# Optimization experiments

Measured on AMD Instinct MI355X. Metric: run time of the kernel, lower is better.

The kernel has to match this reference:

```python
import jax, jax.numpy as jnp
import numpy as np

N_NONZERO = 32      # n_nonzero_coefs
TAU = 0.01
LAMBDA_INIT = -5.0  # reg_coeff = softplus(lambda)


def setup_inputs() -> dict:
    key = jax.random.key(0)
    k1, k2 = jax.random.split(key)
    X = jax.random.normal(k1, (64, 1024, 1024), dtype=jnp.float32)
    y = jax.random.normal(k2, (64, 1024, 1), dtype=jnp.float32)
    return {"X": X, "y": y}


def _omp_fit_forward(X, y):
    # Faithful translation of fit() (omp with hard straight-through top-1)
    # followed by forward() reconstruction D @ coef.
    reg = jax.nn.softplus(jnp.asarray(LAMBDA_INIT, jnp.float32)).astype(X.dtype)
    B, L, A = X.shape
    ones = jnp.ones((B, L, 1), X.dtype)
    Dfull = jnp.concatenate([X, ones], axis=-1)   # [B, L, A+1] (bias column)
    D = Dfull[0]                                   # shared dictionary [L, A+1]
    n_atoms = A + 1
    y2 = y[:, :, 0]                                # [B, L]
    y_det = jax.lax.stop_gradient(y2)
    residuals = y_det
    # Cache selected_D columns incrementally: each column j is dict @ ret_j,
    # identical math to the original's full recompute every iteration.
    selD = jnp.zeros((B, L, N_NONZERO), X.dtype)
    idx_all = []
    nzW = None
    for i in range(N_NONZERO):
        proj = residuals @ D                                      # [B, A+1]
        soft = jax.nn.softmax(jnp.abs(proj) / TAU, axis=-1)
        idx = jnp.argmax(jnp.abs(proj), axis=-1)                  # detached indices
        onehot = jax.nn.one_hot(jnp.argmax(soft, axis=-1), n_atoms, dtype=X.dtype)
        ret = onehot - jax.lax.stop_gradient(soft) + soft         # straight-through
        new_col = ret @ D.T                                       # [B, L]
        selD = selD.at[:, :, i].set(new_col)
        Di = selD[:, :, :i + 1]                                   # [B, L, i+1]
        DTy = jnp.einsum('blk,bl->bk', Di, y2)[..., None]         # [B, i+1, 1]
        DTD = jnp.einsum('blk,blj->bkj', Di, Di) + reg * jnp.eye(i + 1, dtype=X.dtype)
        nzW = jnp.linalg.solve(DTD, DTy)                          # [B, i+1, 1]
        residuals = y_det - jnp.einsum('blk,bk->bl', Di, nzW[..., 0])
        idx_all.append(idx)
    indices = jnp.stack(idx_all, axis=1)                          # [B, K] int
    W = jnp.zeros((B, n_atoms), X.dtype).at[jnp.arange(B)[:, None], indices].set(nzW[..., 0])
    # forward(): bmm(dict_with_bias, coef)
    recon = jnp.einsum('bla,ba->bl', Dfull, W)[..., None]         # [B, L, 1]
    return recon


def reference(X, y):
    return _omp_fit_forward(X, y)
```

## Files before the change

### kernel.cpp

```cpp
#include <hip/hip_runtime.h>
#include <math.h>

#define NATOMS   1025
#define GSTRIDE  1040
#define GELEMS   (1025*GSTRIDE)
#define NNZ      32
#define NBATCH   64
#define REGL     0.0067153485f

#define DPPF(x, ctrl) __int_as_float(__builtin_amdgcn_update_dpp(0, __float_as_int(x), (ctrl), 0xF, 0xF, false))

__device__ __forceinline__ float wave_max64(float x) {
    x = fmaxf(x, DPPF(x, 0x111));
    x = fmaxf(x, DPPF(x, 0x112));
    x = fmaxf(x, DPPF(x, 0x114));
    x = fmaxf(x, DPPF(x, 0x118));
    x = fmaxf(x, DPPF(x, 0x142));
    x = fmaxf(x, DPPF(x, 0x143));
    return __int_as_float(__builtin_amdgcn_readlane(__float_as_int(x), 63));
}
__device__ __forceinline__ float wave_sum64(float x) {
    x += DPPF(x, 0x111);
    x += DPPF(x, 0x112);
    x += DPPF(x, 0x114);
    x += DPPF(x, 0x118);
    x += DPPF(x, 0x142);
    x += DPPF(x, 0x143);
    return __int_as_float(__builtin_amdgcn_readlane(__float_as_int(x), 63));
}

__global__ __launch_bounds__(256)
void gramprojy_kernel(const float* __restrict__ X0, const float* __restrict__ y,
                      float* __restrict__ Gout, float* __restrict__ PY,
                      int kLen, int nsplit) {
    __shared__ float lds[8192];
    const int tid = threadIdx.x;

    if ((int)blockIdx.z < nsplit) {
        const int bx = blockIdx.x, by = blockIdx.y, bz = blockIdx.z;
        if (by < bx) return;
        float* As = lds;
        float* Bs = lds + 4096;
        const int a0 = bx * 128, b0 = by * 128;
        float* __restrict__ Gp = Gout + (size_t)bz * GELEMS;
        const int tx = tid & 15;
        const int ty = tid >> 4;
        const int lr = tid >> 5;
        const int lc = (tid & 31) * 4;
        const bool aIn = (a0 + 128) <= 1024;
        const bool bIn = (b0 + 128) <= 1024;

        float acc[8][8];
#pragma unroll
        for (int m = 0; m < 8; ++m)
#pragma unroll
            for (int n = 0; n < 8; ++n) acc[m][n] = 0.0f;

        const int kBase = bz * kLen;
        for (int kc = 0; kc < kLen; kc += 32) {
#pragma unroll
            for (int rr = 0; rr < 4; ++rr) {
                const int r = lr + rr * 8;
                const int l = kBase + kc + r;
                if (aIn) {
                    *(float4*)&As[r * 128 + lc] = *(const float4*)&X0[(size_t)l * 1024 + a0 + lc];
                } else {
#pragma unroll
                    for (int k = 0; k < 4; ++k) {
                        const int col = a0 + lc + k;
                        As[r * 128 + lc + k] = (col < 1024) ? X0[(size_t)l * 1024 + col]
                                                            : (col == 1024 ? 1.0f : 0.0f);
                    }
                }
                if (bIn) {
                    *(float4*)&Bs[r * 128 + lc] = *(const float4*)&X0[(size_t)l * 1024 + b0 + lc];
                } else {
#pragma unroll
                    for (int k = 0; k < 4; ++k) {
                        const int col = b0 + lc + k;
                        Bs[r * 128 + lc + k] = (col < 1024) ? X0[(size_t)l * 1024 + col]
                                                            : (col == 1024 ? 1.0f : 0.0f);
                    }
                }
            }
            __syncthreads();
#pragma unroll 8
            for (int l = 0; l < 32; ++l) {
                float4 a01 = *(const float4*)&As[l * 128 + ty * 8];
                float4 a23 = *(const float4*)&As[l * 128 + ty * 8 + 4];
                float4 bA  = *(const float4*)&Bs[l * 128 + tx * 4];
                float4 bB  = *(const float4*)&Bs[l * 128 + 64 + tx * 4];
                float am[8] = {a01.x, a01.y, a01.z, a01.w, a23.x, a23.y, a23.z, a23.w};
                float bn[8] = {bA.x, bA.y, bA.z, bA.w, bB.x, bB.y, bB.z, bB.w};
#pragma unroll
                for (int m = 0; m < 8; ++m)
#pragma unroll
                    for (int n = 0; n < 8; ++n)
                        acc[m][n] += am[m] * bn[n];
            }
            __syncthreads();
        }

#pragma unroll
        for (int m = 0; m < 8; ++m) {
            const int a = a0 + ty * 8 + m;
            if (a >= NATOMS) continue;
            const int bAc = b0 + tx * 4;
            const int bBc = b0 + 64 + tx * 4;
            if (bAc < GSTRIDE) {
                *(float4*)&Gp[(size_t)a * GSTRIDE + bAc] =
                    make_float4(acc[m][0], acc[m][1], acc[m][2], acc[m][3]);
            }
            if (bBc < GSTRIDE) {
                *(float4*)&Gp[(size_t)a * GSTRIDE + bBc] =
                    make_float4(acc[m][4], acc[m][5], acc[m][6], acc[m][7]);
            }
        }
    } else {
        const int pw = blockIdx.y * 9 + blockIdx.x;
        if (pw >= 68) return;
        const int a0 = (pw % 17) * 64;
        const int b0 = (pw / 17) * 16;
        float* Ds = lds;
        float* Ys = lds + 2048;
        const int tx = tid & 15;
        const int ty = tid >> 4;
        const bool aIn = (a0 + 64) <= 1024;

        float acc[4] = {0.0f, 0.0f, 0.0f, 0.0f};

        for (int kc = 0; kc < 1024; kc += 32) {
            {
                const int r  = tid >> 4;
                const int c4 = (tid & 15) * 4;
#pragma unroll
                for (int rr = 0; rr < 2; ++rr) {
                    const int row = r + rr * 16;
                    const int l = kc + row;
                    if (aIn) {
                        *(float4*)&Ds[row * 64 + c4] = *(const float4*)&X0[(size_t)l * 1024 + a0 + c4];
                    } else {
#pragma unroll
                        for (int k = 0; k < 4; ++k) {
                            const int col = a0 + c4 + k;
                            Ds[row * 64 + c4 + k] = (col < 1024) ? X0[(size_t)l * 1024 + col]
                                                                 : (col == 1024 ? 1.0f : 0.0f);
                        }
                    }
                }
            }
            for (int e = tid; e < 512; e += 256) {
                const int l = e & 31, bb = e >> 5;
                Ys[l * 17 + bb] = y[(size_t)(b0 + bb) * 1024 + kc + l];
            }
            __syncthreads();
#pragma unroll 8
            for (int l = 0; l < 32; ++l) {
                const float yv = Ys[l * 17 + ty];
                float4 dv = *(const float4*)&Ds[l * 64 + tx * 4];
                acc[0] += yv * dv.x; acc[1] += yv * dv.y;
                acc[2] += yv * dv.z; acc[3] += yv * dv.w;
            }
            __syncthreads();
        }
        const int a = a0 + tx * 4;
        if (a < GSTRIDE) {
            *(float4*)&PY[(size_t)(b0 + ty) * GSTRIDE + a] =
                make_float4(acc[0], acc[1], acc[2], acc[3]);
        }
    }
}

__global__ __launch_bounds__(256)
void combine_kernel(const float* __restrict__ Gp, float* __restrict__ G,
                    float* __restrict__ diagG, int nsplit) {
    int tt = blockIdx.x, bx = 0;
    while (tt >= 9 - bx) { tt -= 9 - bx; ++bx; }
    const int by = bx + tt;
    const int yq = blockIdx.y;
    const int tid = threadIdx.x;
    for (int rep = 0; rep < 16; ++rep) {
        const int idx = yq * 4096 + rep * 256 + tid;
        const int r = idx >> 7, c = idx & 127;
        const int a = bx * 128 + r, b = by * 128 + c;
        if (a > 1024 || b > 1024) continue;
        float s = 0.0f;
        for (int z = 0; z < nsplit; ++z)
            s += Gp[(size_t)z * GELEMS + (size_t)a * GSTRIDE + b];
        G[(size_t)a * GSTRIDE + b] = s;
        G[(size_t)b * GSTRIDE + a] = s;
        if (a == b) diagG[a] = s;
    }
}

__global__ __launch_bounds__(512)
void omp_kernel(const float* __restrict__ G, const float* __restrict__ PY,
                const float* __restrict__ diagG,
                int* __restrict__ idxOut, float* __restrict__ wOut) {
    __shared__ float rowsLds[NNZ][GSTRIDE];
    __shared__ float pyLds[1040];
    __shared__ float diagLds[1040];
    __shared__ float Ainv[32][33];
    __shared__ float wv[32], rhs[32], uvb[32];
    __shared__ int   selIdx[32];
    __shared__ float redV[8];
    __shared__ int   redI[8];
    __shared__ float sc_dinv;

    const int b = blockIdx.x, tid = threadIdx.x;
    const int lane = tid & 63, wid = tid >> 6;

    {
        float4 z4 = make_float4(0.f, 0.f, 0.f, 0.f);
        float4* rz = (float4*)rowsLds;
        for (int u = tid; u < NNZ * GSTRIDE / 4; u += 512) rz[u] = z4;
        if (tid < 32) { wv[tid] = 0.f; rhs[tid] = 0.f; uvb[tid] = 0.f; }
        for (int u = tid; u < 32 * 33; u += 512) ((float*)Ainv)[u] = 0.f;
        const float* pyg = PY + (size_t)b * GSTRIDE;
        for (int u = tid; u < 1040; u += 512) pyLds[u] = pyg[u];
        for (int u = tid; u < 1025; u += 512) diagLds[u] = diagG[u];
    }
    __syncthreads();

    float p0 = pyLds[2 * tid], p1 = pyLds[2 * tid + 1];
    float p2 = (tid == 511) ? pyLds[1024] : 0.0f;

    {
        float best = fabsf(p0); int bidx = 2 * tid;
        { float v = fabsf(p1); if (v > best) { best = v; bidx = 2 * tid + 1; } }
        if (tid == 511) { float v = fabsf(p2); if (v > best) { best = v; bidx = 1024; } }
        const float wmax = wave_max64(best);
        const unsigned long long mask = __ballot(best == wmax);
        const int fl = __ffsll((unsigned long long)mask) - 1;
        const int widx = __builtin_amdgcn_readlane(bidx, fl);
        if (lane == 0) { redV[wid] = wmax; redI[wid] = widx; }
    }
    __syncthreads();

    for (int i = 0; i < NNZ; ++i) {
        float bv_ = redV[0]; int sel = redI[0];
#pragma unroll
        for (int q = 1; q < 8; ++q) {
            if (redV[q] > bv_ || (redV[q] == bv_ && redI[q] < sel)) {
                bv_ = redV[q]; sel = redI[q];
            }
        }
        const float pysel = pyLds[sel];

        float2 rv = make_float2(0.f, 0.f);
        float rv2 = 0.f;
        const float* __restrict__ grow = G + (size_t)sel * GSTRIDE;
        if (i < NNZ - 1) {
            rv = *(const float2*)(grow + 2 * tid);
            if (tid == 511) rv2 = grow[1024];
        }

        if (wid == 0) {
            float bvl = 0.0f, rl = 0.0f;
            if (lane < 32) { bvl = rowsLds[lane][sel]; rl = rhs[lane]; }
            const int lr_ = lane & 31;
            float u0 = 0.f, u1 = 0.f, u2 = 0.f, u3 = 0.f;
#pragma unroll
            for (int m = 0; m < 32; m += 4) {
                u0 = fmaf(Ainv[lr_][m + 0], rowsLds[m + 0][sel], u0);
                u1 = fmaf(Ainv[lr_][m + 1], rowsLds[m + 1][sel], u1);
                u2 = fmaf(Ainv[lr_][m + 2], rowsLds[m + 2][sel], u2);
                u3 = fmaf(Ainv[lr_][m + 3], rowsLds[m + 3][sel], u3);
            }
            const float uacc = (u0 + u1) + (u2 + u3);
            const float t = wave_sum64(bvl * uacc);
            const float s = wave_sum64(rl * uacc);
            const float dinv = 1.0f / (diagLds[sel] + REGL - t);
            const float beta = dinv * (pysel - s);
            if (lane < 32) {
                uvb[lane] = (lane == i) ? -1.0f : uacc;
                wv[lane]  = (lane == i) ? beta  : wv[lane] - uacc * beta;
            }
            if (lane == 0) { selIdx[i] = sel; rhs[i] = pysel; sc_dinv = dinv; }
        }
        __syncthreads();
        if (i == NNZ - 1) break;

        {
            const float dcur = sc_dinv;
            const int e0 = 2 * tid, j0 = e0 >> 5, k0 = e0 & 31;
            Ainv[j0][k0] = fmaf(uvb[j0] * uvb[k0], dcur, Ainv[j0][k0]);
            const int e1 = 2 * tid + 1, j1 = e1 >> 5, k1 = e1 & 31;
            Ainv[j1][k1] = fmaf(uvb[j1] * uvb[k1], dcur, Ainv[j1][k1]);
        }

        const float beta = wv[i];
        float z0 = -rv.x, z1 = -rv.y, z2 = -rv2;
        for (int jb = 0; jb < NNZ; jb += 8) {
            if (jb >= i) break;
#pragma unroll
            for (int jj = 0; jj < 8; ++jj) {
                const int j = jb + jj;
                const float uj = uvb[j];
                z0 = fmaf(uj, rowsLds[j][2 * tid],     z0);
                z1 = fmaf(uj, rowsLds[j][2 * tid + 1], z1);
                if (tid == 511) z2 = fmaf(uj, rowsLds[j][1024], z2);
            }
        }
        p0 = fmaf(beta, z0, p0);
        p1 = fmaf(beta, z1, p1);
        if (tid == 511) p2 = fmaf(beta, z2, p2);

        rowsLds[i][2 * tid]     = rv.x;
        rowsLds[i][2 * tid + 1] = rv.y;
        if (tid == 511) rowsLds[i][1024] = rv2;

        {
            float best = fabsf(p0); int bidx = 2 * tid;
            { float v = fabsf(p1); if (v > best) { best = v; bidx = 2 * tid + 1; } }
            if (tid == 511) { float v = fabsf(p2); if (v > best) { best = v; bidx = 1024; } }
            const float wmax = wave_max64(best);
            const unsigned long long mask = __ballot(best == wmax);
            const int fl = __ffsll((unsigned long long)mask) - 1;
            const int widx = __builtin_amdgcn_readlane(bidx, fl);
            if (lane == 0) { redV[wid] = wmax; redI[wid] = widx; }
        }
        __syncthreads();
    }

    if (tid < NNZ) {
        idxOut[b * NNZ + tid] = selIdx[tid];
        wOut[b * NNZ + tid] = wv[tid];
    }
}

__global__ __launch_bounds__(256)
void recon_kernel(const float* __restrict__ X, const int* __restrict__ idxIn,
                  const float* __restrict__ wIn, float* __restrict__ out) {
    __shared__ float4 Wd4[260];
    const int b = blockIdx.x >> 3, chunk = blockIdx.x & 7;
    const int tid = threadIdx.x, lane = tid & 63, wid = tid >> 6;
    float* Wd = (float*)Wd4;
    for (int u = tid; u < 1040; u += 256) Wd[u] = 0.0f;
    __syncthreads();
    if (tid == 0) {
#pragma unroll
        for (int i = 0; i < NNZ; ++i) Wd[idxIn[b * NNZ + i]] = wIn[b * NNZ + i];
    }
    __syncthreads();
    const float wOne = Wd[1024];
    const float* Xb = X + (size_t)b * 1024 * 1024;

    for (int rr = wid; rr < 128; rr += 4) {
        const int r = chunk * 128 + rr;
        const float4* xr = (const float4*)(Xb + (size_t)r * 1024);
        float acc = 0.0f;
#pragma unroll
        for (int q = 0; q < 4; ++q) {
            float4 x = xr[q * 64 + lane];
            float4 w = Wd4[q * 64 + lane];
            acc += x.x * w.x + x.y * w.y + x.z * w.z + x.w * w.w;
        }
        acc = wave_sum64(acc);
        if (lane == 0) out[(size_t)b * 1024 + r] = acc + wOne;
    }
}

extern "C" void kernel_launch(void* const* d_in, const int* in_sizes, int n_in,
                              void* d_out, int out_size, void* d_ws, size_t ws_size,
                              hipStream_t stream) {
    const float* X = (const float*)d_in[0];
    const float* y = (const float*)d_in[1];
    float* out = (float*)d_out;
    float* ws = (float*)d_ws;

    const size_t need4 = ((size_t)GELEMS * 5 + 64 * GSTRIDE + NBATCH * NNZ * 2 + 2048) * sizeof(float);
    const int nsplit = (ws_size >= need4) ? 4 : 1;
    const int kLen = 1024 / nsplit;

    float* Gp = ws;
    float* G  = ws + (size_t)GELEMS * nsplit;
    float* PY = G + (size_t)GELEMS;
    float* wOut = PY + (size_t)64 * GSTRIDE;
    int* idxOut = (int*)(wOut + NBATCH * NNZ);
    float* diagG = (float*)(idxOut + NBATCH * NNZ);

    gramprojy_kernel<<<dim3(9, 9, nsplit + 1), 256, 0, stream>>>(X, y, Gp, PY, kLen, nsplit);
    combine_kernel<<<dim3(45, 4), 256, 0, stream>>>(Gp, G, diagG, nsplit);
    omp_kernel<<<NBATCH, 512, 0, stream>>>(G, PY, diagG, idxOut, wOut);
    recon_kernel<<<NBATCH * 8, 256, 0, stream>>>(X, idxOut, wOut, out);
}
```

Before: 218.7 us.

## Fuse split-K Gram reduction into OMP row gathers and sparsify reconstruction

Removes the combine kernel. The OMP kernel now sums the split-K partial Gram tiles on the fly, only for the rows it selects and the diagonal, and uses the upper-triangle tile layout to pick an offset. The reconstruction kernel now gathers only the 32 selected columns of X per row, with one thread per row, instead of a dense 1024-wide dot product. This saves a full Gram pass and most of the X read traffic in recon. In exchange, the OMP row loads become nsplit-fold and partly strided (column reads of a row), and the recon gathers from X are uncoalesced.

New measurement: 301.8 us. +38.0%, slower.

```diff
diff --git a/kernel.cpp b/kernel.cpp
--- a/kernel.cpp
+++ b/kernel.cpp
@@ -171,32 +171,9 @@
     }
 }
 
-__global__ __launch_bounds__(256)
-void combine_kernel(const float* __restrict__ Gp, float* __restrict__ G,
-                    float* __restrict__ diagG, int nsplit) {
-    int tt = blockIdx.x, bx = 0;
-    while (tt >= 9 - bx) { tt -= 9 - bx; ++bx; }
-    const int by = bx + tt;
-    const int yq = blockIdx.y;
-    const int tid = threadIdx.x;
-    for (int rep = 0; rep < 16; ++rep) {
-        const int idx = yq * 4096 + rep * 256 + tid;
-        const int r = idx >> 7, c = idx & 127;
-        const int a = bx * 128 + r, b = by * 128 + c;
-        if (a > 1024 || b > 1024) continue;
-        float s = 0.0f;
-        for (int z = 0; z < nsplit; ++z)
-            s += Gp[(size_t)z * GELEMS + (size_t)a * GSTRIDE + b];
-        G[(size_t)a * GSTRIDE + b] = s;
-        G[(size_t)b * GSTRIDE + a] = s;
-        if (a == b) diagG[a] = s;
-    }
-}
-
 __global__ __launch_bounds__(512)
-void omp_kernel(const float* __restrict__ G, const float* __restrict__ PY,
-                const float* __restrict__ diagG,
-                int* __restrict__ idxOut, float* __restrict__ wOut) {
+void omp_kernel(const float* __restrict__ Gp, const float* __restrict__ PY,
+                int nsplit, int* __restrict__ idxOut, float* __restrict__ wOut) {
     __shared__ float rowsLds[NNZ][GSTRIDE];
     __shared__ float pyLds[1040];
     __shared__ float diagLds[1040];
@@ -218,16 +195,25 @@
         for (int u = tid; u < 32 * 33; u += 512) ((float*)Ainv)[u] = 0.f;
         const float* pyg = PY + (size_t)b * GSTRIDE;
         for (int u = tid; u < 1040; u += 512) pyLds[u] = pyg[u];
-        for (int u = tid; u < 1025; u += 512) diagLds[u] = diagG[u];
+        float d0 = 0.f, d1 = 0.f, d2 = 0.f;
+        for (int z = 0; z < nsplit; ++z) {
+            const float* gz = Gp + (size_t)z * GELEMS;
+            d0 += gz[(size_t)tid * GSTRIDE + tid];
+            d1 += gz[(size_t)(tid + 512) * GSTRIDE + (tid + 512)];
+            if (tid == 511) d2 += gz[(size_t)1024 * GSTRIDE + 1024];
+        }
+        diagLds[tid] = d0;
+        diagLds[tid + 512] = d1;
+        if (tid == 511) diagLds[1024] = d2;
     }
     __syncthreads();
 
-    float p0 = pyLds[2 * tid], p1 = pyLds[2 * tid + 1];
+    float p0 = pyLds[tid], p1 = pyLds[tid + 512];
     float p2 = (tid == 511) ? pyLds[1024] : 0.0f;
 
     {
-        float best = fabsf(p0); int bidx = 2 * tid;
-        { float v = fabsf(p1); if (v > best) { best = v; bidx = 2 * tid + 1; } }
+        float best = fabsf(p0); int bidx = tid;
+        { float v = fabsf(p1); if (v > best) { best = v; bidx = tid + 512; } }
         if (tid == 511) { float v = fabsf(p2); if (v > best) { best = v; bidx = 1024; } }
         const float wmax = wave_max64(best);
         const unsigned long long mask = __ballot(best == wmax);
@@ -247,12 +233,25 @@
         }
         const float pysel = pyLds[sel];
 
-        float2 rv = make_float2(0.f, 0.f);
-        float rv2 = 0.f;
-        const float* __restrict__ grow = G + (size_t)sel * GSTRIDE;
+        float r0 = 0.f, r1 = 0.f, r2 = 0.f;
         if (i < NNZ - 1) {
-            rv = *(const float2*)(grow + 2 * tid);
-            if (tid == 511) rv2 = grow[1024];
+            const int st = sel >> 7;
+            {
+                const int a = tid;
+                const size_t off = (st <= (a >> 7)) ? ((size_t)sel * GSTRIDE + a)
+                                                    : ((size_t)a * GSTRIDE + sel);
+                for (int z = 0; z < nsplit; ++z) r0 += Gp[(size_t)z * GELEMS + off];
+            }
+            {
+                const int a = tid + 512;
+                const size_t off = (st <= (a >> 7)) ? ((size_t)sel * GSTRIDE + a)
+                                                    : ((size_t)a * GSTRIDE + sel);
+                for (int z = 0; z < nsplit; ++z) r1 += Gp[(size_t)z * GELEMS + off];
+            }
+            if (tid == 511) {
+                const size_t off = (size_t)sel * GSTRIDE + 1024;
+                for (int z = 0; z < nsplit; ++z) r2 += Gp[(size_t)z * GELEMS + off];
+            }
         }
 
         if (wid == 0) {
@@ -290,15 +289,15 @@
         }
 
         const float beta = wv[i];
-        float z0 = -rv.x, z1 = -rv.y, z2 = -rv2;
+        float z0 = -r0, z1 = -r1, z2 = -r2;
         for (int jb = 0; jb < NNZ; jb += 8) {
             if (jb >= i) break;
 #pragma unroll
             for (int jj = 0; jj < 8; ++jj) {
                 const int j = jb + jj;
                 const float uj = uvb[j];
-                z0 = fmaf(uj, rowsLds[j][2 * tid],     z0);
-                z1 = fmaf(uj, rowsLds[j][2 * tid + 1], z1);
+                z0 = fmaf(uj, rowsLds[j][tid],       z0);
+                z1 = fmaf(uj, rowsLds[j][tid + 512], z1);
                 if (tid == 511) z2 = fmaf(uj, rowsLds[j][1024], z2);
             }
         }
@@ -306,13 +305,13 @@
         p1 = fmaf(beta, z1, p1);
         if (tid == 511) p2 = fmaf(beta, z2, p2);
 
-        rowsLds[i][2 * tid]     = rv.x;
-        rowsLds[i][2 * tid + 1] = rv.y;
-        if (tid == 511) rowsLds[i][1024] = rv2;
+        rowsLds[i][tid]       = r0;
+        rowsLds[i][tid + 512] = r1;
+        if (tid == 511) rowsLds[i][1024] = r2;
 
         {
-            float best = fabsf(p0); int bidx = 2 * tid;
-            { float v = fabsf(p1); if (v > best) { best = v; bidx = 2 * tid + 1; } }
+            float best = fabsf(p0); int bidx = tid;
+            { float v = fabsf(p1); if (v > best) { best = v; bidx = tid + 512; } }
             if (tid == 511) { float v = fabsf(p2); if (v > best) { best = v; bidx = 1024; } }
             const float wmax = wave_max64(best);
             const unsigned long long mask = __ballot(best == wmax);
@@ -332,33 +331,42 @@
 __global__ __launch_bounds__(256)
 void recon_kernel(const float* __restrict__ X, const int* __restrict__ idxIn,
                   const float* __restrict__ wIn, float* __restrict__ out) {
-    __shared__ float4 Wd4[260];
-    const int b = blockIdx.x >> 3, chunk = blockIdx.x & 7;
-    const int tid = threadIdx.x, lane = tid & 63, wid = tid >> 6;
-    float* Wd = (float*)Wd4;
-    for (int u = tid; u < 1040; u += 256) Wd[u] = 0.0f;
+    __shared__ float Wd[1025];
+    __shared__ float wval[NNZ];
+    __shared__ int   widx[NNZ];
+    __shared__ float biasS;
+    const int b = blockIdx.x >> 2, chunk = blockIdx.x & 3;
+    const int tid = threadIdx.x;
+    for (int u = tid; u < 1025; u += 256) Wd[u] = 0.0f;
     __syncthreads();
     if (tid == 0) {
 #pragma unroll
         for (int i = 0; i < NNZ; ++i) Wd[idxIn[b * NNZ + i]] = wIn[b * NNZ + i];
+        float bias = 0.0f;
+#pragma unroll
+        for (int i = 0; i < NNZ; ++i) {
+            const int gi = idxIn[b * NNZ + i];
+            const float v = Wd[gi];
+            Wd[gi] = 0.0f;
+            const bool isOnes = (gi == 1024);
+            if (isOnes) bias += v;
+            widx[i] = isOnes ? 0 : gi;
+            wval[i] = isOnes ? 0.0f : v;
+        }
+        biasS = bias;
     }
     __syncthreads();
-    const float wOne = Wd[1024];
-    const float* Xb = X + (size_t)b * 1024 * 1024;
-
-    for (int rr = wid; rr < 128; rr += 4) {
-        const int r = chunk * 128 + rr;
-        const float4* xr = (const float4*)(Xb + (size_t)r * 1024);
-        float acc = 0.0f;
-#pragma unroll
-        for (int q = 0; q < 4; ++q) {
-            float4 x = xr[q * 64 + lane];
-            float4 w = Wd4[q * 64 + lane];
-            acc += x.x * w.x + x.y * w.y + x.z * w.z + x.w * w.w;
-        }
-        acc = wave_sum64(acc);
-        if (lane == 0) out[(size_t)b * 1024 + r] = acc + wOne;
-    }
+    const int l = chunk * 256 + tid;
+    const float* __restrict__ xr = X + (size_t)b * 1024 * 1024 + (size_t)l * 1024;
+    float a0 = biasS, a1 = 0.f, a2 = 0.f, a3 = 0.f;
+#pragma unroll
+    for (int i = 0; i < NNZ; i += 4) {
+        a0 = fmaf(xr[widx[i + 0]], wval[i + 0], a0);
+        a1 = fmaf(xr[widx[i + 1]], wval[i + 1], a1);
+        a2 = fmaf(xr[widx[i + 2]], wval[i + 2], a2);
+        a3 = fmaf(xr[widx[i + 3]], wval[i + 3], a3);
+    }
+    out[(size_t)b * 1024 + l] = (a0 + a1) + (a2 + a3);
 }
 
 extern "C" void kernel_launch(void* const* d_in, const int* in_sizes, int n_in,
@@ -369,19 +377,16 @@
     float* out = (float*)d_out;
     float* ws = (float*)d_ws;
 
-    const size_t need4 = ((size_t)GELEMS * 5 + 64 * GSTRIDE + NBATCH * NNZ * 2 + 2048) * sizeof(float);
+    const size_t need4 = ((size_t)GELEMS * 4 + 64 * GSTRIDE + NBATCH * NNZ * 2 + 64) * sizeof(float);
     const int nsplit = (ws_size >= need4) ? 4 : 1;
     const int kLen = 1024 / nsplit;
 
     float* Gp = ws;
-    float* G  = ws + (size_t)GELEMS * nsplit;
-    float* PY = G + (size_t)GELEMS;
+    float* PY = ws + (size_t)GELEMS * nsplit;
     float* wOut = PY + (size_t)64 * GSTRIDE;
     int* idxOut = (int*)(wOut + NBATCH * NNZ);
-    float* diagG = (float*)(idxOut + NBATCH * NNZ);
 
     gramprojy_kernel<<<dim3(9, 9, nsplit + 1), 256, 0, stream>>>(X, y, Gp, PY, kLen, nsplit);
-    combine_kernel<<<dim3(45, 4), 256, 0, stream>>>(Gp, G, diagG, nsplit);
-    omp_kernel<<<NBATCH, 512, 0, stream>>>(G, PY, diagG, idxOut, wOut);
-    recon_kernel<<<NBATCH * 8, 256, 0, stream>>>(X, idxOut, wOut, out);
-}
+    omp_kernel<<<NBATCH, 512, 0, stream>>>(Gp, PY, nsplit, idxOut, wOut);
+    recon_kernel<<<NBATCH * 4, 256, 0, stream>>>(X, idxOut, wOut, out);
+}
```
